# Optimization experiments

Measured on AMD Instinct MI355X. Metric: run time of the kernel, lower is better.

## Reference

```python
import jax, jax.numpy as jnp
import numpy as np

B, S, E = 2, 8192, 128


def setup_inputs() -> dict:
    key = jax.random.key(0)
    ks = jax.random.split(key, 7)
    sc = 1.0 / np.sqrt(E)
    return {
        "x": jax.random.normal(ks[0], (B, S, E), dtype=jnp.float32),
        "Wq": jax.random.normal(ks[1], (E, E), dtype=jnp.float32) * sc,
        "bq": jax.random.normal(ks[2], (E,), dtype=jnp.float32) * 0.01,
        "Wk": jax.random.normal(ks[3], (E, E), dtype=jnp.float32) * sc,
        "bk": jax.random.normal(ks[4], (E,), dtype=jnp.float32) * 0.01,
        "Wv": jax.random.normal(ks[5], (E, E), dtype=jnp.float32) * sc,
        "bv": jax.random.normal(ks[6], (E,), dtype=jnp.float32) * 0.01,
    }


def reference(x, Wq, bq, Wk, bk, Wv, bv):
    # x: [B, S, E]. Conv1d(k=1) == per-slice linear: out[b,s,o] = sum_e W[o,e] x[b,s,e] + b[o]
    embed_dim = x.shape[-1]
    Q = jnp.einsum("bse,oe->bso", x, Wq) + bq  # [B, S, E]
    K = jnp.einsum("bse,oe->bso", x, Wk) + bk
    V = jnp.einsum("bse,oe->bso", x, Wv) + bv
    scores = jnp.einsum("bsd,btd->bst", Q, K) / jnp.sqrt(
        jnp.asarray(embed_dim, dtype=x.dtype)
    )  # [B, S, S]
    A = jax.nn.softmax(scores, axis=-1)
    # torch: out = bmm(V^T_as[B,E,S], A^T)[.transpose] == sum_t A[b,s,t] V[b,t,e]
    out = jnp.einsum("bst,bte->bse", A, V)  # [B, S, E]
    return out
```

## Files before the change

kernel.cpp:

```cpp
#include <hip/hip_runtime.h>
#include <math.h>

#define NB 2
#define NS 8192
#define NE 128
#define NROWS (NB * NS)

typedef __attribute__((ext_vector_type(8))) short s8v;
typedef __attribute__((ext_vector_type(16))) float fx16;
typedef __attribute__((ext_vector_type(2))) unsigned int u2v;
typedef __attribute__((address_space(1))) const unsigned char as1c;
typedef __attribute__((address_space(3))) unsigned char as3t;

static __device__ __forceinline__ unsigned int pkbf(float a, float b) {
    unsigned int ua = __float_as_uint(a), ub = __float_as_uint(b);
    ua += 0x7FFFu + ((ua >> 16) & 1u);
    ub += 0x7FFFu + ((ub >> 16) & 1u);
    return (ua >> 16) | (ub & 0xFFFF0000u);
}

static __device__ __forceinline__ unsigned int cvtpk(float a, float b) {
    unsigned int r;
    asm("v_cvt_pk_bf16_f32 %0, %1, %2" : "=v"(r) : "v"(a), "v"(b));
    return r;
}

static __device__ __forceinline__ void split8(const float* p, uint4& H, uint4& L) {
    float4 a = *(const float4*)p;
    float4 b = *(const float4*)(p + 4);
    unsigned int h0 = cvtpk(a.x, a.y), h1 = cvtpk(a.z, a.w);
    unsigned int h2 = cvtpk(b.x, b.y), h3 = cvtpk(b.z, b.w);
    H = make_uint4(h0, h1, h2, h3);
    float l0 = a.x - __uint_as_float(h0 << 16);
    float l1 = a.y - __uint_as_float(h0 & 0xFFFF0000u);
    float l2 = a.z - __uint_as_float(h1 << 16);
    float l3 = a.w - __uint_as_float(h1 & 0xFFFF0000u);
    float l4 = b.x - __uint_as_float(h2 << 16);
    float l5 = b.y - __uint_as_float(h2 & 0xFFFF0000u);
    float l6 = b.z - __uint_as_float(h3 << 16);
    float l7 = b.w - __uint_as_float(h3 & 0xFFFF0000u);
    L = make_uint4(cvtpk(l0, l1), cvtpk(l2, l3), cvtpk(l4, l5), cvtpk(l6, l7));
}

__global__ __launch_bounds__(256, 4)
void split_kernel(const float* __restrict__ x,
                  const float* __restrict__ Wq, const float* __restrict__ Wk,
                  const float* __restrict__ Wv,
                  unsigned short* __restrict__ xh, unsigned short* __restrict__ xl,
                  unsigned short* __restrict__ WhS, unsigned short* __restrict__ WlS)
{
    const int bid = blockIdx.x;
    if (bid < 1024) {
        const int i = (bid * 256 + threadIdx.x) * 8;
        uint4 H, L;
        split8(&x[i], H, L);
        *(uint4*)&xh[i] = H;
        *(uint4*)&xl[i] = L;
    } else {
        const int tid = (bid - 1024) * 256 + threadIdx.x;
        const int mat = tid >> 11;
        const int rem = tid & 2047;
        const int r = rem >> 4, g = rem & 15;
        const float* W = (mat == 0) ? Wq : (mat == 1) ? Wk : Wv;
        uint4 H, L;
        split8(&W[r * 128 + g * 8], H, L);
        const int gs = g ^ (r & 7);
        *(uint4*)&WhS[mat * 16384 + r * 128 + gs * 8] = H;
        *(uint4*)&WlS[mat * 16384 + r * 128 + gs * 8] = L;
    }
}

__global__ __launch_bounds__(256, 2)
void qkv_kernel(const unsigned short* __restrict__ xh,
                const unsigned short* __restrict__ xl,
                const unsigned short* __restrict__ WhS,
                const unsigned short* __restrict__ WlS,
                const float* __restrict__ bq, const float* __restrict__ bk,
                const float* __restrict__ bv,
                unsigned short* __restrict__ qkv)
{
    __shared__ unsigned short xhL[64 * 128];
    __shared__ unsigned short xlL[64 * 128];
    __shared__ unsigned short WhL[64 * 128];
    __shared__ unsigned short WlL[64 * 128];

    const int t    = threadIdx.x;
    const int rblk = blockIdx.x * 64;
    const int mat  = blockIdx.y;
    const int o0   = blockIdx.z * 64;

    const float* bias = (mat == 0) ? bq : (mat == 1) ? bk : bv;
    unsigned short* out = qkv + (size_t)mat * NROWS * NE;
    const float osc = (mat == 0) ? 0.1275174460620886f : 1.0f;

    const int w = t >> 6, lane = t & 63, lq = lane & 31, h = lane >> 5;

    if (w < 2) {
        const unsigned short* src = (w == 0) ? xh : xl;
        unsigned short* dst = (w == 0) ? xhL : xlL;
        const int rb4 = lane >> 4;
        const int cg  = lane & 15;
        #pragma unroll
        for (int i = 0; i < 16; ++i) {
            const int row = 4 * i + rb4;
            const int c   = cg ^ (row & 7);
            __builtin_amdgcn_global_load_lds(
                (as1c*)(src + (size_t)(rblk + row) * NE + c * 8),
                (as3t*)(dst + i * 512 + lane * 8), 16, 0, 0);
        }
    } else {
        const unsigned short* src = ((w == 2) ? WhS : WlS) + mat * 16384 + o0 * 128;
        unsigned short* dst = (w == 2) ? WhL : WlL;
        #pragma unroll
        for (int i = 0; i < 16; ++i) {
            __builtin_amdgcn_global_load_lds(
                (as1c*)(src + i * 512 + lane * 8),
                (as3t*)(dst + i * 512 + lane * 8), 16, 0, 0);
        }
    }
    __syncthreads();

    const int rloc = (w & 1) * 32;
    const int ot   = w >> 1;

    s8v xhf[8], xlf[8], whf[8], wlf[8];
    #pragma unroll
    for (int s = 0; s < 8; ++s) {
        const int cx = ((s * 2 + h) ^ (lq & 7)) * 8;
        xhf[s] = *(const s8v*)&xhL[(rloc + lq) * 128 + cx];
        xlf[s] = *(const s8v*)&xlL[(rloc + lq) * 128 + cx];
        whf[s] = *(const s8v*)&WhL[(ot * 32 + lq) * 128 + cx];
        wlf[s] = *(const s8v*)&WlL[(ot * 32 + lq) * 128 + cx];
    }

    fx16 acc;
    #pragma unroll
    for (int i = 0; i < 16; ++i) acc[i] = 0.f;

    #pragma unroll
    for (int s = 0; s < 8; ++s) {
        if (mat != 2) {
            acc = __builtin_amdgcn_mfma_f32_32x32x16_bf16(whf[s], xhf[s], acc, 0, 0, 0);
            acc = __builtin_amdgcn_mfma_f32_32x32x16_bf16(whf[s], xlf[s], acc, 0, 0, 0);
            acc = __builtin_amdgcn_mfma_f32_32x32x16_bf16(wlf[s], xhf[s], acc, 0, 0, 0);
        } else {
            acc = __builtin_amdgcn_mfma_f32_32x32x16_bf16(xhf[s], whf[s], acc, 0, 0, 0);
            acc = __builtin_amdgcn_mfma_f32_32x32x16_bf16(xlf[s], whf[s], acc, 0, 0, 0);
            acc = __builtin_amdgcn_mfma_f32_32x32x16_bf16(xhf[s], wlf[s], acc, 0, 0, 0);
        }
    }

    __syncthreads();
    unsigned short* TB = xhL;

    if (mat != 2) {
        #pragma unroll
        for (int g = 0; g < 4; ++g) {
            const int ob = o0 + ot * 32 + 4 * h + 8 * g;
            float4 bb = *(const float4*)&bias[ob];
            float v0 = (acc[4 * g + 0] + bb.x) * osc;
            float v1 = (acc[4 * g + 1] + bb.y) * osc;
            float v2 = (acc[4 * g + 2] + bb.z) * osc;
            float v3 = (acc[4 * g + 3] + bb.w) * osc;
            *(uint2*)&TB[(rloc + lq) * 72 + ot * 32 + 4 * h + 8 * g] =
                make_uint2(pkbf(v0, v1), pkbf(v2, v3));
        }
        __syncthreads();
        #pragma unroll
        for (int it = 0; it < 2; ++it) {
            const int r2 = it * 32 + (t >> 3);
            const int c2 = (t & 7) * 8;
            uint4 vv = *(const uint4*)&TB[r2 * 72 + c2];
            *(uint4*)&out[(size_t)(rblk + r2) * NE + o0 + c2] = vv;
        }
    } else {
        const float bv_ = bias[o0 + ot * 32 + lq];
        #pragma unroll
        for (int g = 0; g < 4; ++g) {
            float v0 = acc[4 * g + 0] + bv_;
            float v1 = acc[4 * g + 1] + bv_;
            float v2 = acc[4 * g + 2] + bv_;
            float v3 = acc[4 * g + 3] + bv_;
            *(uint2*)&TB[(ot * 32 + lq) * 72 + rloc + 4 * h + 8 * g] =
                make_uint2(pkbf(v0, v1), pkbf(v2, v3));
        }
        __syncthreads();
        const int bb_ = rblk >> 13;
        #pragma unroll
        for (int it = 0; it < 2; ++it) {
            const int d2 = it * 32 + (t >> 3);
            const int kc = (t & 7) * 8;
            uint4 vv = *(const uint4*)&TB[d2 * 72 + kc];
            *(uint4*)&out[(((size_t)(bb_ * NE + o0 + d2)) << 13)
                          + (rblk & (NS - 1)) + kc] = vv;
        }
    }
}

__global__ __launch_bounds__(256, 2)
void attn_kernel(const unsigned short* __restrict__ qkv,
                 _Float16* __restrict__ pd,
                 _Float16* __restrict__ pw,
                 float* __restrict__ ml)
{
    __shared__ unsigned short kbuf[2][64 * 128];
    __shared__ unsigned short vbuf[2][64 * 128];

    const int t  = threadIdx.x;
    const int id = blockIdx.x;
    const int ks = id & 3;
    const int b  = (id >> 2) & 1;
    const int T  = id >> 3;

    const unsigned short* Qg = qkv;
    const unsigned short* Kg = qkv + (size_t)NROWS * NE;
    const unsigned short* Vb = qkv + (size_t)2 * NROWS * NE + ((size_t)b << 20);

    const int w = t >> 6, lane = t & 63, lq = lane & 31, h = lane >> 5;
    const int qbw = b * NS + T * 128 + w * 32;
    const size_t kvb = (size_t)b * NS * NE;
    const int kq0 = ks * 2048;

    s8v qf[8];
    #pragma unroll
    for (int s = 0; s < 8; ++s)
        qf[s] = *(const s8v*)(Qg + (size_t)(qbw + lq) * NE + s * 16 + h * 8);

    fx16 acc[4];
    #pragma unroll
    for (int dt = 0; dt < 4; ++dt)
        #pragma unroll
        for (int i = 0; i < 16; ++i) acc[dt][i] = 0.f;

    float l = 0.f;

    const unsigned short* gptr[8];
    if (w < 2) {
        #pragma unroll
        for (int j = 0; j < 8; ++j) {
            int i = 8 * w + j;
            int keyl = 4 * i + (lane >> 4);
            int c = (lane & 15) ^ (keyl & 7);
            gptr[j] = Kg + kvb + (size_t)(kq0 + keyl) * NE + c * 8;
        }
    } else {
        #pragma unroll
        for (int j = 0; j < 8; ++j) {
            int i = 8 * (w - 2) + j;
            int d = 8 * i + (lane >> 3);
            int g = (lane & 7) ^ (d & 7);
            gptr[j] = Vb + ((size_t)d << 13) + kq0 + g * 8;
        }
    }
    const int gstride = (w < 2) ? 64 * NE : 64;

    auto stageK = [&](int bufi) {
        if (w < 2) {
            #pragma unroll
            for (int j = 0; j < 8; ++j) {
                __builtin_amdgcn_global_load_lds((as1c*)gptr[j],
                    (as3t*)&kbuf[bufi][(8 * w + j) * 512], 16, 0, 0);
                gptr[j] += gstride;
            }
        }
    };
    auto stageV = [&](int bufi) {
        if (w >= 2) {
            #pragma unroll
            for (int j = 0; j < 8; ++j) {
                __builtin_amdgcn_global_load_lds((as1c*)gptr[j],
                    (as3t*)&vbuf[bufi][(8 * (w - 2) + j) * 512], 16, 0, 0);
                gptr[j] += gstride;
            }
        }
    };

    const int swz = (lq & 7) * 8;

    auto gemm1 = [&](fx16 (&st)[2], int bufi) {
        #pragma unroll
        for (int mt = 0; mt < 2; ++mt)
            #pragma unroll
            for (int i = 0; i < 16; ++i) st[mt][i] = 0.f;
        __builtin_amdgcn_s_setprio(1);
        #pragma unroll
        for (int s = 0; s < 8; ++s) {
            int co = ((s * 2 + h) * 8) ^ swz;
            s8v a0 = *(const s8v*)&kbuf[bufi][lq * 128 + co];
            s8v a1 = *(const s8v*)&kbuf[bufi][(32 + lq) * 128 + co];
            st[0] = __builtin_amdgcn_mfma_f32_32x32x16_bf16(a0, qf[s], st[0], 0, 0, 0);
            st[1] = __builtin_amdgcn_mfma_f32_32x32x16_bf16(a1, qf[s], st[1], 0, 0, 0);
        }
        __builtin_amdgcn_s_setprio(0);
    };

#define PEX(st, i) (st[(i) >> 4][(i) & 15])
    auto smax = [&](fx16 (&st)[2]) {
        float a0s = 0.f, a1s = 0.f, a2s = 0.f, a3s = 0.f;
        #pragma unroll
        for (int i = 0; i < 32; i += 4) {
            PEX(st, i)     = __builtin_amdgcn_exp2f(PEX(st, i));
            PEX(st, i + 1) = __builtin_amdgcn_exp2f(PEX(st, i + 1));
            PEX(st, i + 2) = __builtin_amdgcn_exp2f(PEX(st, i + 2));
            PEX(st, i + 3) = __builtin_amdgcn_exp2f(PEX(st, i + 3));
            a0s += PEX(st, i); a1s += PEX(st, i + 1);
            a2s += PEX(st, i + 2); a3s += PEX(st, i + 3);
        }
        float lsum = (a0s + a1s) + (a2s + a3s);
        lsum += __shfl_xor(lsum, 32);
        l += lsum;
    };

    auto gemm2 = [&](fx16 (&st)[2], int bufi) {
        #pragma unroll
        for (int s2 = 0; s2 < 4; ++s2) {
            unsigned int P0 = cvtpk(PEX(st, s2 * 8 + 0), PEX(st, s2 * 8 + 1));
            unsigned int P1 = cvtpk(PEX(st, s2 * 8 + 2), PEX(st, s2 * 8 + 3));
            unsigned int P2 = cvtpk(PEX(st, s2 * 8 + 4), PEX(st, s2 * 8 + 5));
            unsigned int P3 = cvtpk(PEX(st, s2 * 8 + 6), PEX(st, s2 * 8 + 7));
            u2v r02 = __builtin_amdgcn_permlane32_swap(P0, P2, false, false);
            u2v r13 = __builtin_amdgcn_permlane32_swap(P1, P3, false, false);
            union { unsigned int u[4]; s8v v; } pf;
            pf.u[0] = r02.x;
            pf.u[1] = r13.x;
            pf.u[2] = r02.y;
            pf.u[3] = r13.y;
            int go = ((s2 * 2 + h) * 8) ^ swz;
            __builtin_amdgcn_s_setprio(1);
            #pragma unroll
            for (int dt = 0; dt < 4; ++dt) {
                s8v vf = *(const s8v*)&vbuf[bufi][(lq + 32 * dt) * 64 + go];
                acc[dt] = __builtin_amdgcn_mfma_f32_32x32x16_bf16(pf.v, vf, acc[dt], 0, 0, 0);
            }
            __builtin_amdgcn_s_setprio(0);
        }
    };

    stageK(0);
    stageV(0);
    __syncthreads();
    fx16 stA[2], stB[2];
    gemm1(stA, 0);
    stageK(1);
    __syncthreads();

    for (int r2 = 0; r2 < 16; ++r2) {
        const bool notlast = (r2 < 15);
        if (notlast) stageK(0);
        stageV(1);
        smax(stA);
        gemm1(stB, 1);
        gemm2(stA, 0);
        __syncthreads();
        if (notlast) {
            stageK(1);
            stageV(0);
        }
        smax(stB);
        if (notlast) gemm1(stA, 0);
        gemm2(stB, 1);
        __syncthreads();
    }
#undef PEX

    if (lane < 32)
        ml[(size_t)(qbw + lq) * 4 + ks] = l;

    float invl = 1.0f / l;
    _Float16* P = (ks < 2) ? pd : pw;
    const int slot = (ks & 1) * 128;
    #pragma unroll
    for (int rg = 0; rg < 16; ++rg) {
        int row = (rg & 3) + 8 * (rg >> 2) + 4 * h;
        float sc = __shfl(invl, row);
        size_t rb = (size_t)(qbw + row) * 256 + slot;
        #pragma unroll
        for (int dt = 0; dt < 4; ++dt)
            P[rb + lq + 32 * dt] = (_Float16)(acc[dt][rg] * sc);
    }
}

__global__ __launch_bounds__(256, 2)
void merge_kernel(const _Float16* __restrict__ pw,
                  const float* __restrict__ ml,
                  float* __restrict__ outp)
{
    const int gi = blockIdx.x * 256 + threadIdx.x;
    const int q = gi >> 4, d0 = (gi & 15) * 8;
    const _Float16* pd = (const _Float16*)outp;

    uint4 u0 = *(const uint4*)&pd[(size_t)q * 256 + d0];
    uint4 u1 = *(const uint4*)&pd[(size_t)q * 256 + 128 + d0];
    uint4 u2 = *(const uint4*)&pw[(size_t)q * 256 + d0];
    uint4 u3 = *(const uint4*)&pw[(size_t)q * 256 + 128 + d0];
    float l0 = ml[q * 4 + 0], l1 = ml[q * 4 + 1];
    float l2 = ml[q * 4 + 2], l3 = ml[q * 4 + 3];

    float inv = 1.f / (l0 + l1 + l2 + l3);
    float a0 = l0 * inv, a1 = l1 * inv, a2 = l2 * inv, a3 = l3 * inv;

    union { uint4 u; _Float16 hh[8]; } c0, c1, c2, c3;
    c0.u = u0; c1.u = u1; c2.u = u2; c3.u = u3;
    float ov[8];
    #pragma unroll
    for (int e = 0; e < 8; ++e)
        ov[e] = (float)c0.hh[e] * a0 + (float)c1.hh[e] * a1 +
                (float)c2.hh[e] * a2 + (float)c3.hh[e] * a3;

    *(float4*)&outp[(size_t)q * 128 + d0]     = *(float4*)&ov[0];
    *(float4*)&outp[(size_t)q * 128 + d0 + 4] = *(float4*)&ov[4];
}

extern "C" void kernel_launch(void* const* d_in, const int* in_sizes, int n_in,
                              void* d_out, int out_size, void* d_ws, size_t ws_size,
                              hipStream_t stream)
{
    const float* x  = (const float*)d_in[0];
    const float* Wq = (const float*)d_in[1];
    const float* bq = (const float*)d_in[2];
    const float* Wk = (const float*)d_in[3];
    const float* bk = (const float*)d_in[4];
    const float* Wv = (const float*)d_in[5];
    const float* bv = (const float*)d_in[6];
    float* out = (float*)d_out;

    unsigned char* ws = (unsigned char*)d_ws;
    unsigned short* qkv = (unsigned short*)ws;
    _Float16* pw = (_Float16*)(ws + (size_t)3 * NROWS * NE * 2);
    float* mlp = (float*)(ws + (size_t)3 * NROWS * NE * 2
                             + (size_t)NROWS * 256 * 2);
    unsigned char* ws2 = ws + (size_t)3 * NROWS * NE * 2
                            + (size_t)NROWS * 256 * 2 + (size_t)NROWS * 16;
    unsigned short* xh  = (unsigned short*)ws2;
    unsigned short* xl  = xh + (size_t)NROWS * NE;
    unsigned short* WhS = xl + (size_t)NROWS * NE;
    unsigned short* WlS = WhS + 3 * NE * NE;

    split_kernel<<<1048, 256, 0, stream>>>(x, Wq, Wk, Wv, xh, xl, WhS, WlS);

    dim3 g1(NROWS / 64, 3, 2);
    qkv_kernel<<<g1, 256, 0, stream>>>(xh, xl, WhS, WlS, bq, bk, bv, qkv);

    attn_kernel<<<512, 256, 0, stream>>>(qkv, (_Float16*)d_out, pw, mlp);
    merge_kernel<<<1024, 256, 0, stream>>>(pw, mlp, out);
}
```

Measured before the change: 163.8 us.

## Fuse x bf16 split into QKV projection and loop all outputs per block

The separate split of x into bf16 hi/lo halves is folded into the QKV projection kernel, which now converts x directly from fp32 into shared memory. This removes the xh/xl workspace round trip. Each block now walks all six output tiles (three matrices times two column halves), reusing its x fragments and prefetching the next weight tile while computing the current one. The grid shrinks from 1536 blocks to 256, which lowers parallelism and makes each block's work more serial.

```diff
diff --git a/kernel.cpp b/kernel.cpp
--- a/kernel.cpp
+++ b/kernel.cpp
@@ -43,36 +43,24 @@
 }
 
 __global__ __launch_bounds__(256, 4)
-void split_kernel(const float* __restrict__ x,
-                  const float* __restrict__ Wq, const float* __restrict__ Wk,
-                  const float* __restrict__ Wv,
-                  unsigned short* __restrict__ xh, unsigned short* __restrict__ xl,
-                  unsigned short* __restrict__ WhS, unsigned short* __restrict__ WlS)
+void splitW_kernel(const float* __restrict__ Wq, const float* __restrict__ Wk,
+                   const float* __restrict__ Wv,
+                   unsigned short* __restrict__ WhS, unsigned short* __restrict__ WlS)
 {
-    const int bid = blockIdx.x;
-    if (bid < 1024) {
-        const int i = (bid * 256 + threadIdx.x) * 8;
-        uint4 H, L;
-        split8(&x[i], H, L);
-        *(uint4*)&xh[i] = H;
-        *(uint4*)&xl[i] = L;
-    } else {
-        const int tid = (bid - 1024) * 256 + threadIdx.x;
-        const int mat = tid >> 11;
-        const int rem = tid & 2047;
-        const int r = rem >> 4, g = rem & 15;
-        const float* W = (mat == 0) ? Wq : (mat == 1) ? Wk : Wv;
-        uint4 H, L;
-        split8(&W[r * 128 + g * 8], H, L);
-        const int gs = g ^ (r & 7);
-        *(uint4*)&WhS[mat * 16384 + r * 128 + gs * 8] = H;
-        *(uint4*)&WlS[mat * 16384 + r * 128 + gs * 8] = L;
-    }
+    const int tid = blockIdx.x * 256 + threadIdx.x;
+    const int mat = tid >> 11;
+    const int rem = tid & 2047;
+    const int r = rem >> 4, g = rem & 15;
+    const float* W = (mat == 0) ? Wq : (mat == 1) ? Wk : Wv;
+    uint4 H, L;
+    split8(&W[r * 128 + g * 8], H, L);
+    const int gs = g ^ (r & 7);
+    *(uint4*)&WhS[mat * 16384 + r * 128 + gs * 8] = H;
+    *(uint4*)&WlS[mat * 16384 + r * 128 + gs * 8] = L;
 }
 
 __global__ __launch_bounds__(256, 2)
-void qkv_kernel(const unsigned short* __restrict__ xh,
-                const unsigned short* __restrict__ xl,
+void qkv_kernel(const float* __restrict__ x,
                 const unsigned short* __restrict__ WhS,
                 const unsigned short* __restrict__ WlS,
                 const float* __restrict__ bq, const float* __restrict__ bk,
@@ -83,116 +71,124 @@
     __shared__ unsigned short xlL[64 * 128];
     __shared__ unsigned short WhL[64 * 128];
     __shared__ unsigned short WlL[64 * 128];
+    __shared__ unsigned short TB[64 * 72];
 
     const int t    = threadIdx.x;
     const int rblk = blockIdx.x * 64;
-    const int mat  = blockIdx.y;
-    const int o0   = blockIdx.z * 64;
-
-    const float* bias = (mat == 0) ? bq : (mat == 1) ? bk : bv;
-    unsigned short* out = qkv + (size_t)mat * NROWS * NE;
-    const float osc = (mat == 0) ? 0.1275174460620886f : 1.0f;
-
     const int w = t >> 6, lane = t & 63, lq = lane & 31, h = lane >> 5;
 
-    if (w < 2) {
-        const unsigned short* src = (w == 0) ? xh : xl;
-        unsigned short* dst = (w == 0) ? xhL : xlL;
-        const int rb4 = lane >> 4;
-        const int cg  = lane & 15;
-        #pragma unroll
-        for (int i = 0; i < 16; ++i) {
-            const int row = 4 * i + rb4;
-            const int c   = cg ^ (row & 7);
-            __builtin_amdgcn_global_load_lds(
-                (as1c*)(src + (size_t)(rblk + row) * NE + c * 8),
-                (as3t*)(dst + i * 512 + lane * 8), 16, 0, 0);
-        }
-    } else {
-        const unsigned short* src = ((w == 2) ? WhS : WlS) + mat * 16384 + o0 * 128;
-        unsigned short* dst = (w == 2) ? WhL : WlL;
-        #pragma unroll
-        for (int i = 0; i < 16; ++i) {
-            __builtin_amdgcn_global_load_lds(
-                (as1c*)(src + i * 512 + lane * 8),
-                (as3t*)(dst + i * 512 + lane * 8), 16, 0, 0);
-        }
-    }
+    auto stageW = [&](int mo) {
+        const int mat = mo >> 1;
+        const unsigned short* hs = WhS + mat * 16384 + (mo & 1) * 8192;
+        const unsigned short* ls = WlS + mat * 16384 + (mo & 1) * 8192;
+        #pragma unroll
+        for (int p = 0; p < 4; ++p) {
+            __builtin_amdgcn_global_load_lds((as1c*)(hs + p * 2048 + t * 8),
+                (as3t*)&WhL[p * 2048 + t * 8], 16, 0, 0);
+            __builtin_amdgcn_global_load_lds((as1c*)(ls + p * 2048 + t * 8),
+                (as3t*)&WlL[p * 2048 + t * 8], 16, 0, 0);
+        }
+    };
+
+    {
+        const int row = t >> 2, cg0 = (t & 3) * 4;
+        #pragma unroll
+        for (int g = 0; g < 4; ++g) {
+            uint4 H, L;
+            split8(&x[(size_t)(rblk + row) * NE + (cg0 + g) * 8], H, L);
+            const int gs = (cg0 + g) ^ (row & 7);
+            *(uint4*)&xhL[row * 128 + gs * 8] = H;
+            *(uint4*)&xlL[row * 128 + gs * 8] = L;
+        }
+    }
+    stageW(0);
     __syncthreads();
 
     const int rloc = (w & 1) * 32;
     const int ot   = w >> 1;
 
-    s8v xhf[8], xlf[8], whf[8], wlf[8];
+    s8v xhf[8], xlf[8];
     #pragma unroll
     for (int s = 0; s < 8; ++s) {
         const int cx = ((s * 2 + h) ^ (lq & 7)) * 8;
         xhf[s] = *(const s8v*)&xhL[(rloc + lq) * 128 + cx];
         xlf[s] = *(const s8v*)&xlL[(rloc + lq) * 128 + cx];
-        whf[s] = *(const s8v*)&WhL[(ot * 32 + lq) * 128 + cx];
-        wlf[s] = *(const s8v*)&WlL[(ot * 32 + lq) * 128 + cx];
-    }
-
-    fx16 acc;
-    #pragma unroll
-    for (int i = 0; i < 16; ++i) acc[i] = 0.f;
-
-    #pragma unroll
-    for (int s = 0; s < 8; ++s) {
+    }
+
+    for (int mo = 0; mo < 6; ++mo) {
+        const int mat = mo >> 1, o0 = (mo & 1) * 64;
+        const float* bias = (mat == 0) ? bq : (mat == 1) ? bk : bv;
+        unsigned short* out = qkv + (size_t)mat * NROWS * NE;
+        const float osc = (mat == 0) ? 0.1275174460620886f : 1.0f;
+
+        s8v whf[8], wlf[8];
+        #pragma unroll
+        for (int s = 0; s < 8; ++s) {
+            const int cx = ((s * 2 + h) ^ (lq & 7)) * 8;
+            whf[s] = *(const s8v*)&WhL[(ot * 32 + lq) * 128 + cx];
+            wlf[s] = *(const s8v*)&WlL[(ot * 32 + lq) * 128 + cx];
+        }
+        __syncthreads();
+        if (mo < 5) stageW(mo + 1);
+
+        fx16 acc;
+        #pragma unroll
+        for (int i = 0; i < 16; ++i) acc[i] = 0.f;
+
+        #pragma unroll
+        for (int s = 0; s < 8; ++s) {
+            if (mat != 2) {
+                acc = __builtin_amdgcn_mfma_f32_32x32x16_bf16(whf[s], xhf[s], acc, 0, 0, 0);
+                acc = __builtin_amdgcn_mfma_f32_32x32x16_bf16(whf[s], xlf[s], acc, 0, 0, 0);
+                acc = __builtin_amdgcn_mfma_f32_32x32x16_bf16(wlf[s], xhf[s], acc, 0, 0, 0);
+            } else {
+                acc = __builtin_amdgcn_mfma_f32_32x32x16_bf16(xhf[s], whf[s], acc, 0, 0, 0);
+                acc = __builtin_amdgcn_mfma_f32_32x32x16_bf16(xlf[s], whf[s], acc, 0, 0, 0);
+                acc = __builtin_amdgcn_mfma_f32_32x32x16_bf16(xhf[s], wlf[s], acc, 0, 0, 0);
+            }
+        }
+
         if (mat != 2) {
-            acc = __builtin_amdgcn_mfma_f32_32x32x16_bf16(whf[s], xhf[s], acc, 0, 0, 0);
-            acc = __builtin_amdgcn_mfma_f32_32x32x16_bf16(whf[s], xlf[s], acc, 0, 0, 0);
-            acc = __builtin_amdgcn_mfma_f32_32x32x16_bf16(wlf[s], xhf[s], acc, 0, 0, 0);
+            #pragma unroll
+            for (int g = 0; g < 4; ++g) {
+                const int ob = o0 + ot * 32 + 4 * h + 8 * g;
+                float4 bb = *(const float4*)&bias[ob];
+                float v0 = (acc[4 * g + 0] + bb.x) * osc;
+                float v1 = (acc[4 * g + 1] + bb.y) * osc;
+                float v2 = (acc[4 * g + 2] + bb.z) * osc;
+                float v3 = (acc[4 * g + 3] + bb.w) * osc;
+                *(uint2*)&TB[(rloc + lq) * 72 + ot * 32 + 4 * h + 8 * g] =
+                    make_uint2(pkbf(v0, v1), pkbf(v2, v3));
+            }
+            __syncthreads();
+            #pragma unroll
+            for (int it = 0; it < 2; ++it) {
+                const int r2 = it * 32 + (t >> 3);
+                const int c2 = (t & 7) * 8;
+                uint4 vv = *(const uint4*)&TB[r2 * 72 + c2];
+                *(uint4*)&out[(size_t)(rblk + r2) * NE + o0 + c2] = vv;
+            }
         } else {
-            acc = __builtin_amdgcn_mfma_f32_32x32x16_bf16(xhf[s], whf[s], acc, 0, 0, 0);
-            acc = __builtin_amdgcn_mfma_f32_32x32x16_bf16(xlf[s], whf[s], acc, 0, 0, 0);
-            acc = __builtin_amdgcn_mfma_f32_32x32x16_bf16(xhf[s], wlf[s], acc, 0, 0, 0);
-        }
-    }
-
-    __syncthreads();
-    unsigned short* TB = xhL;
-
-    if (mat != 2) {
-        #pragma unroll
-        for (int g = 0; g < 4; ++g) {
-            const int ob = o0 + ot * 32 + 4 * h + 8 * g;
-            float4 bb = *(const float4*)&bias[ob];
-            float v0 = (acc[4 * g + 0] + bb.x) * osc;
-            float v1 = (acc[4 * g + 1] + bb.y) * osc;
-            float v2 = (acc[4 * g + 2] + bb.z) * osc;
-            float v3 = (acc[4 * g + 3] + bb.w) * osc;
-            *(uint2*)&TB[(rloc + lq) * 72 + ot * 32 + 4 * h + 8 * g] =
-                make_uint2(pkbf(v0, v1), pkbf(v2, v3));
-        }
-        __syncthreads();
-        #pragma unroll
-        for (int it = 0; it < 2; ++it) {
-            const int r2 = it * 32 + (t >> 3);
-            const int c2 = (t & 7) * 8;
-            uint4 vv = *(const uint4*)&TB[r2 * 72 + c2];
-            *(uint4*)&out[(size_t)(rblk + r2) * NE + o0 + c2] = vv;
-        }
-    } else {
-        const float bv_ = bias[o0 + ot * 32 + lq];
-        #pragma unroll
-        for (int g = 0; g < 4; ++g) {
-            float v0 = acc[4 * g + 0] + bv_;
-            float v1 = acc[4 * g + 1] + bv_;
-            float v2 = acc[4 * g + 2] + bv_;
-            float v3 = acc[4 * g + 3] + bv_;
-            *(uint2*)&TB[(ot * 32 + lq) * 72 + rloc + 4 * h + 8 * g] =
-                make_uint2(pkbf(v0, v1), pkbf(v2, v3));
-        }
-        __syncthreads();
-        const int bb_ = rblk >> 13;
-        #pragma unroll
-        for (int it = 0; it < 2; ++it) {
-            const int d2 = it * 32 + (t >> 3);
-            const int kc = (t & 7) * 8;
-            uint4 vv = *(const uint4*)&TB[d2 * 72 + kc];
-            *(uint4*)&out[(((size_t)(bb_ * NE + o0 + d2)) << 13)
-                          + (rblk & (NS - 1)) + kc] = vv;
+            const float bv_ = bias[o0 + ot * 32 + lq];
+            #pragma unroll
+            for (int g = 0; g < 4; ++g) {
+                float v0 = acc[4 * g + 0] + bv_;
+                float v1 = acc[4 * g + 1] + bv_;
+                float v2 = acc[4 * g + 2] + bv_;
+                float v3 = acc[4 * g + 3] + bv_;
+                *(uint2*)&TB[(ot * 32 + lq) * 72 + rloc + 4 * h + 8 * g] =
+                    make_uint2(pkbf(v0, v1), pkbf(v2, v3));
+            }
+            __syncthreads();
+            const int bb_ = rblk >> 13;
+            #pragma unroll
+            for (int it = 0; it < 2; ++it) {
+                const int d2 = it * 32 + (t >> 3);
+                const int kc = (t & 7) * 8;
+                uint4 vv = *(const uint4*)&TB[d2 * 72 + kc];
+                *(uint4*)&out[(((size_t)(bb_ * NE + o0 + d2)) << 13)
+                              + (rblk & (NS - 1)) + kc] = vv;
+            }
         }
     }
 }
@@ -429,17 +425,13 @@
     _Float16* pw = (_Float16*)(ws + (size_t)3 * NROWS * NE * 2);
     float* mlp = (float*)(ws + (size_t)3 * NROWS * NE * 2
                              + (size_t)NROWS * 256 * 2);
-    unsigned char* ws2 = ws + (size_t)3 * NROWS * NE * 2
-                            + (size_t)NROWS * 256 * 2 + (size_t)NROWS * 16;
-    unsigned short* xh  = (unsigned short*)ws2;
-    unsigned short* xl  = xh + (size_t)NROWS * NE;
-    unsigned short* WhS = xl + (size_t)NROWS * NE;
+    unsigned short* WhS = (unsigned short*)(ws + (size_t)3 * NROWS * NE * 2
+                             + (size_t)NROWS * 256 * 2 + (size_t)NROWS * 16);
     unsigned short* WlS = WhS + 3 * NE * NE;
 
-    split_kernel<<<1048, 256, 0, stream>>>(x, Wq, Wk, Wv, xh, xl, WhS, WlS);
-
-    dim3 g1(NROWS / 64, 3, 2);
-    qkv_kernel<<<g1, 256, 0, stream>>>(xh, xl, WhS, WlS, bq, bk, bv, qkv);
+    splitW_kernel<<<24, 256, 0, stream>>>(Wq, Wk, Wv, WhS, WlS);
+
+    qkv_kernel<<<NROWS / 64, 256, 0, stream>>>(x, WhS, WlS, bq, bk, bv, qkv);
 
     attn_kernel<<<512, 256, 0, stream>>>(qkv, (_Float16*)d_out, pw, mlp);
     merge_kernel<<<1024, 256, 0, stream>>>(pw, mlp, out);
```

After: 159.0 us. 1.03x faster.
